# Performance work log

Measured on AMD Instinct MI355X. Metric: run time of the kernel, lower is better.

## Reference

```python
import jax, jax.numpy as jnp
import numpy as np

DIM = 768
HEADS = 12
EXPERTS = 8
HID = 3072  # dim * moe_mlp_ratio(=4)
TOP_K = 2
LN_EPS = 1e-5


def _layer_norm(x, g, b):
    mu = x.mean(-1, keepdims=True)
    var = ((x - mu) ** 2).mean(-1, keepdims=True)
    return (x - mu) * jax.lax.rsqrt(var + LN_EPS) * g + b


def setup_inputs() -> dict:
    key = jax.random.key(0)
    ks = jax.random.split(key, 16)
    s = 0.02
    return {
        "x": jax.random.normal(ks[0], (8, 196, DIM), jnp.float32),
        "ln1_g": jnp.ones((DIM,), jnp.float32),
        "ln1_b": jnp.zeros((DIM,), jnp.float32),
        "qkv_w": jax.random.normal(ks[1], (DIM, 3 * DIM), jnp.float32) * s,
        "qkv_b": jnp.zeros((3 * DIM,), jnp.float32),
        "proj_w": jax.random.normal(ks[2], (DIM, DIM), jnp.float32) * s,
        "proj_b": jnp.zeros((DIM,), jnp.float32),
        "ln2_g": jnp.ones((DIM,), jnp.float32),
        "ln2_b": jnp.zeros((DIM,), jnp.float32),
        "gate_w": jax.random.normal(ks[3], (DIM, EXPERTS), jnp.float32) * s,
        "w1": jax.random.normal(ks[4], (EXPERTS, DIM, HID), jnp.float32) * s,
        "b1": jnp.zeros((EXPERTS, HID), jnp.float32),
        "w2": jax.random.normal(ks[5], (EXPERTS, HID, DIM), jnp.float32) * s,
        "b2": jnp.zeros((EXPERTS, DIM), jnp.float32),
    }


def _attention(x, qkv_w, qkv_b, proj_w, proj_b):
    B, N, C = x.shape
    hd = C // HEADS
    qkv = (x @ qkv_w + qkv_b).reshape(B, N, 3, HEADS, hd).transpose(2, 0, 3, 1, 4)
    q, k, v = qkv[0], qkv[1], qkv[2]  # [B,H,N,hd]
    attn = jax.nn.softmax(jnp.einsum("bhnd,bhmd->bhnm", q, k) * (hd ** -0.5), axis=-1)
    o = jnp.einsum("bhnm,bhmd->bhnd", attn, v).transpose(0, 2, 1, 3).reshape(B, N, C)
    return o @ proj_w + proj_b


def _moe_mlp(xn, gate_w, w1, b1, w2, b2):
    # xn: [T, D]; noisy top-k gate in eval mode (no noise)
    T = xn.shape[0]
    logits = xn @ gate_w                                   # [T, E]
    top_logits, top_idx = jax.lax.top_k(logits, TOP_K)     # [T, k]
    top_gates = jax.nn.softmax(top_logits, axis=-1)        # [T, k]
    gates = jnp.zeros((T, EXPERTS), xn.dtype).at[
        jnp.arange(T)[:, None], top_idx
    ].set(top_gates)                                       # [T, E] sparse combine weights
    # dense-masked expert compute (math identical to dispatch: gate=0 tokens contribute 0)
    h = jax.nn.gelu(jnp.einsum("td,edh->teh", xn, w1) + b1, approximate=False)
    y = jnp.einsum("teh,ehd->ted", h, w2) + b2             # [T, E, D]
    return jnp.einsum("ted,te->td", y, gates)


def reference(x, ln1_g, ln1_b, qkv_w, qkv_b, proj_w, proj_b,
              ln2_g, ln2_b, gate_w, w1, b1, w2, b2):
    B, N, C = x.shape
    x = x + _attention(_layer_norm(x, ln1_g, ln1_b), qkv_w, qkv_b, proj_w, proj_b)
    xn = _layer_norm(x, ln2_g, ln2_b).reshape(B * N, C)
    moe_out = _moe_mlp(xn, gate_w, w1, b1, w2, b2).reshape(B, N, C)
    return x + moe_out
```

## Files before the change

kernel.cpp:

```cpp
#include <hip/hip_runtime.h>
#include <hip/hip_bf16.h>
#include <math.h>

#define DIMC 768
#define HEADS 12
#define HD 64
#define EXPERTS 8
#define HID 3072
#define BB 8
#define NN 196
#define TT (BB*NN)
#define CAP_ROWS 4224
#define LN_EPS 1e-5f

typedef float f32x4_t __attribute__((ext_vector_type(4)));
typedef short bf16x8_t __attribute__((ext_vector_type(8)));
typedef unsigned short u16x8_t __attribute__((ext_vector_type(8)));

__device__ __forceinline__ unsigned short f2bf(float f) {
    unsigned int u = __float_as_uint(f);
    u += 0x7FFFu + ((u >> 16) & 1u);
    return (unsigned short)(u >> 16);
}
__device__ __forceinline__ float bf2f(unsigned short u) {
    return __uint_as_float(((unsigned int)u) << 16);
}

__device__ __forceinline__ void gl_lds16(const void* g, void* l) {
    __builtin_amdgcn_global_load_lds(
        (const __attribute__((address_space(1))) unsigned int*)g,
        (__attribute__((address_space(3))) unsigned int*)l, 16, 0, 0);
}

template<int GATE>
__global__ void ln_kernel_t(const float* __restrict__ x, const float* __restrict__ g,
                            const float* __restrict__ b,
                            unsigned short* __restrict__ out_hi,
                            unsigned short* __restrict__ out_lo,
                            const float* __restrict__ gw, int* __restrict__ tok_e,
                            float* __restrict__ tok_g, int* __restrict__ counts) {
    int t = blockIdx.x;
    const float* xr = x + (size_t)t * DIMC;
    int tid = threadIdx.x;
    float v0 = xr[tid], v1 = xr[tid + 256], v2 = xr[tid + 512];
    __shared__ float red[256];
    red[tid] = v0 + v1 + v2;
    __syncthreads();
    for (int off = 128; off > 0; off >>= 1) {
        if (tid < off) red[tid] += red[tid + off];
        __syncthreads();
    }
    float mu = red[0] * (1.0f / DIMC);
    __syncthreads();
    float d0 = v0 - mu, d1 = v1 - mu, d2 = v2 - mu;
    red[tid] = d0*d0 + d1*d1 + d2*d2;
    __syncthreads();
    for (int off = 128; off > 0; off >>= 1) {
        if (tid < off) red[tid] += red[tid + off];
        __syncthreads();
    }
    float rstd = rsqrtf(red[0] * (1.0f / DIMC) + LN_EPS);
    float o0 = d0 * rstd * g[tid]       + b[tid];
    float o1 = d1 * rstd * g[tid + 256] + b[tid + 256];
    float o2 = d2 * rstd * g[tid + 512] + b[tid + 512];
    {
        unsigned short* o = out_hi + (size_t)t * DIMC;
        unsigned short h0 = f2bf(o0), h1 = f2bf(o1), h2 = f2bf(o2);
        o[tid] = h0; o[tid + 256] = h1; o[tid + 512] = h2;
        if (out_lo) {
            unsigned short* ol = out_lo + (size_t)t * DIMC;
            ol[tid]       = f2bf(o0 - bf2f(h0));
            ol[tid + 256] = f2bf(o1 - bf2f(h1));
            ol[tid + 512] = f2bf(o2 - bf2f(h2));
        }
    }
    if (GATE) {
        float p[8];
        const float* g0r = gw + (size_t)tid * 8;
        const float* g1r = gw + ((size_t)tid + 256) * 8;
        const float* g2r = gw + ((size_t)tid + 512) * 8;
        #pragma unroll
        for (int e = 0; e < 8; ++e)
            p[e] = o0 * g0r[e] + o1 * g1r[e] + o2 * g2r[e];
        #pragma unroll
        for (int off = 32; off > 0; off >>= 1)
            #pragma unroll
            for (int e = 0; e < 8; ++e) p[e] += __shfl_xor(p[e], off, 64);
        __shared__ float redw[4][8];
        int lane = tid & 63, w = tid >> 6;
        if (lane == 0) {
            #pragma unroll
            for (int e = 0; e < 8; ++e) redw[w][e] = p[e];
        }
        __syncthreads();
        if (tid == 0) {
            float lg[8];
            #pragma unroll
            for (int e = 0; e < 8; ++e)
                lg[e] = redw[0][e] + redw[1][e] + redw[2][e] + redw[3][e];
            int e0 = 0; float l0 = lg[0];
            #pragma unroll
            for (int e = 1; e < 8; ++e) if (lg[e] > l0) { l0 = lg[e]; e0 = e; }
            int e1 = -1; float l1 = -3e38f;
            #pragma unroll
            for (int e = 0; e < 8; ++e) if (e != e0 && lg[e] > l1) { l1 = lg[e]; e1 = e; }
            float pp = expf(l1 - l0);
            float ga = 1.f / (1.f + pp);
            float gb = pp / (1.f + pp);
            tok_e[t*2] = e0; tok_e[t*2+1] = e1;
            tok_g[t*2] = ga; tok_g[t*2+1] = gb;
            atomicAdd(&counts[e0], 1);
            atomicAdd(&counts[e1], 1);
        }
    }
}

__global__ void attn_mfma_kernel(const float* __restrict__ qkv,
                                 unsigned short* __restrict__ ao_h,
                                 unsigned short* __restrict__ ao_l) {
    __shared__ char psb[64 * 896];
    __shared__ unsigned short QsH[64 * 64], QsL[64 * 64];
    __shared__ unsigned short KsH[64 * 64], KsL[64 * 64];

    int bh = blockIdx.x;
    int b = bh / HEADS, h = bh % HEADS;
    int q0 = blockIdx.y * 64;
    const float* base = qkv + (size_t)b * NN * 2304 + h * 64;

    int tid = threadIdx.x;
    int sr = tid >> 3, sq = tid & 7;
    int lane = tid & 63;
    int wid = tid >> 6;
    int wm = (wid >> 2) * 32;
    int wn = (wid & 3) * 16;
    int lrow = lane & 15;
    int lq = lane >> 4;
    int colb_base = lq * 16;

    {
        int r = sr;
        int n = q0 + r;
        float v[8] = {0.f,0.f,0.f,0.f,0.f,0.f,0.f,0.f};
        if (n < NN) {
            float4 a0 = *(const float4*)(base + (size_t)n * 2304 + sq * 8);
            float4 a1 = *(const float4*)(base + (size_t)n * 2304 + sq * 8 + 4);
            v[0]=a0.x; v[1]=a0.y; v[2]=a0.z; v[3]=a0.w;
            v[4]=a1.x; v[5]=a1.y; v[6]=a1.z; v[7]=a1.w;
        }
        u16x8_t hv, lv;
        #pragma unroll
        for (int t = 0; t < 8; ++t) {
            unsigned short hh = f2bf(v[t]);
            hv[t] = hh; lv[t] = f2bf(v[t] - bf2f(hh));
        }
        int off = r * 128 + ((sq * 16) ^ ((r & 7) << 4));
        *(u16x8_t*)((char*)QsH + off) = hv;
        *(u16x8_t*)((char*)QsL + off) = lv;
    }

    for (int kt = 0; kt < 4; ++kt) {
        int j0 = kt * 64;
        __syncthreads();
        {
            int r = sr;
            int n = j0 + r;
            float v[8] = {0.f,0.f,0.f,0.f,0.f,0.f,0.f,0.f};
            if (n < NN) {
                float4 a0 = *(const float4*)(base + (size_t)n * 2304 + 768 + sq * 8);
                float4 a1 = *(const float4*)(base + (size_t)n * 2304 + 768 + sq * 8 + 4);
                v[0]=a0.x; v[1]=a0.y; v[2]=a0.z; v[3]=a0.w;
                v[4]=a1.x; v[5]=a1.y; v[6]=a1.z; v[7]=a1.w;
            }
            u16x8_t hv, lv;
            #pragma unroll
            for (int t = 0; t < 8; ++t) {
                unsigned short hh = f2bf(v[t]);
                hv[t] = hh; lv[t] = f2bf(v[t] - bf2f(hh));
            }
            int off = r * 128 + ((sq * 16) ^ ((r & 7) << 4));
            *(u16x8_t*)((char*)KsH + off) = hv;
            *(u16x8_t*)((char*)KsL + off) = lv;
        }
        __syncthreads();

        f32x4_t acc[2] = {};
        #pragma unroll
        for (int kk = 0; kk < 2; ++kk) {
            int colb = kk * 64 + colb_base;
            bf16x8_t qh[2], ql[2], kh, kl;
            #pragma unroll
            for (int i = 0; i < 2; ++i) {
                int ra = wm + i * 16 + lrow;
                int oa = ra * 128 + (colb ^ ((ra & 7) << 4));
                qh[i] = *(const bf16x8_t*)((const char*)QsH + oa);
                ql[i] = *(const bf16x8_t*)((const char*)QsL + oa);
            }
            int rb = wn + lrow;
            int ob = rb * 128 + (colb ^ ((rb & 7) << 4));
            kh = *(const bf16x8_t*)((const char*)KsH + ob);
            kl = *(const bf16x8_t*)((const char*)KsL + ob);
            #pragma unroll
            for (int mi = 0; mi < 2; ++mi) {
                acc[mi] = __builtin_amdgcn_mfma_f32_16x16x32_bf16(qh[mi], kh, acc[mi], 0, 0, 0);
                acc[mi] = __builtin_amdgcn_mfma_f32_16x16x32_bf16(qh[mi], kl, acc[mi], 0, 0, 0);
                acc[mi] = __builtin_amdgcn_mfma_f32_16x16x32_bf16(ql[mi], kh, acc[mi], 0, 0, 0);
            }
        }
        int jc = j0 + wn + lrow;
        if (jc < 224) {
            #pragma unroll
            for (int mi = 0; mi < 2; ++mi) {
                #pragma unroll
                for (int j = 0; j < 4; ++j) {
                    int row = wm + mi * 16 + lq * 4 + j;
                    int s = (row & 7) ^ (row >> 3);
                    *(float*)(psb + row * 896 + ((jc * 4) ^ (s << 4))) = acc[mi][j] * 0.125f;
                }
            }
        }
    }
    __syncthreads();

    {
        int i = tid >> 3, l = tid & 7;
        int s = (i & 7) ^ (i >> 3);
        char* prow = psb + i * 896;
        float mx = -1e30f;
        for (int j = l; j < NN; j += 8) mx = fmaxf(mx, *(const float*)(prow + ((j * 4) ^ (s << 4))));
        mx = fmaxf(mx, __shfl_xor(mx, 1, 8));
        mx = fmaxf(mx, __shfl_xor(mx, 2, 8));
        mx = fmaxf(mx, __shfl_xor(mx, 4, 8));
        float sum = 0.f;
        for (int j = l; j < NN; j += 8) {
            float* pp = (float*)(prow + ((j * 4) ^ (s << 4)));
            float e = expf(*pp - mx); *pp = e; sum += e;
        }
        sum += __shfl_xor(sum, 1, 8);
        sum += __shfl_xor(sum, 2, 8);
        sum += __shfl_xor(sum, 4, 8);
        float inv = 1.f / sum;
        for (int j = l; j < NN; j += 8) {
            float* pp = (float*)(prow + ((j * 4) ^ (s << 4)));
            *pp *= inv;
        }
    }

    f32x4_t oacc[2] = {};
    for (int kt = 0; kt < 4; ++kt) {
        int j0 = kt * 64;
        __syncthreads();
        {
            int r = sr;
            int n = j0 + r;
            float v[8] = {0.f,0.f,0.f,0.f,0.f,0.f,0.f,0.f};
            if (n < NN) {
                float4 a0 = *(const float4*)(base + (size_t)n * 2304 + 1536 + sq * 8);
                float4 a1 = *(const float4*)(base + (size_t)n * 2304 + 1536 + sq * 8 + 4);
                v[0]=a0.x; v[1]=a0.y; v[2]=a0.z; v[3]=a0.w;
                v[4]=a1.x; v[5]=a1.y; v[6]=a1.z; v[7]=a1.w;
            }
            #pragma unroll
            for (int t = 0; t < 8; ++t) {
                int d = sq * 8 + t;
                int sw = ((d & 7) ^ (d >> 3)) << 4;
                unsigned short hh = f2bf(v[t]);
                int off = d * 128 + ((r * 2) ^ sw);
                *(unsigned short*)((char*)KsH + off) = hh;
                *(unsigned short*)((char*)KsL + off) = f2bf(v[t] - bf2f(hh));
            }
        }
        __syncthreads();

        int kkmax = (kt == 3) ? 1 : 2;
        for (int kk = 0; kk < kkmax; ++kk) {
            int colb = kk * 64 + colb_base;
            bf16x8_t pah[2], pal[2], vh, vl;
            #pragma unroll
            for (int i = 0; i < 2; ++i) {
                int ra = wm + i * 16 + lrow;
                int s = (ra & 7) ^ (ra >> 3);
                const char* prow = psb + ra * 896;
                int jb = (j0 + kk * 32 + lq * 8) * 4;
                float4 a0 = *(const float4*)(prow + (jb ^ (s << 4)));
                float4 a1 = *(const float4*)(prow + ((jb + 16) ^ (s << 4)));
                float vv[8] = {a0.x,a0.y,a0.z,a0.w,a1.x,a1.y,a1.z,a1.w};
                u16x8_t hv, lv;
                #pragma unroll
                for (int t = 0; t < 8; ++t) {
                    unsigned short hh = f2bf(vv[t]);
                    hv[t] = hh; lv[t] = f2bf(vv[t] - bf2f(hh));
                }
                pah[i] = *(bf16x8_t*)&hv;
                pal[i] = *(bf16x8_t*)&lv;
            }
            int rb = wn + lrow;
            int ob = rb * 128 + (colb ^ (((rb & 7) ^ (rb >> 3)) << 4));
            vh = *(const bf16x8_t*)((const char*)KsH + ob);
            vl = *(const bf16x8_t*)((const char*)KsL + ob);
            #pragma unroll
            for (int mi = 0; mi < 2; ++mi) {
                oacc[mi] = __builtin_amdgcn_mfma_f32_16x16x32_bf16(pah[mi], vh, oacc[mi], 0, 0, 0);
                oacc[mi] = __builtin_amdgcn_mfma_f32_16x16x32_bf16(pah[mi], vl, oacc[mi], 0, 0, 0);
                oacc[mi] = __builtin_amdgcn_mfma_f32_16x16x32_bf16(pal[mi], vh, oacc[mi], 0, 0, 0);
            }
        }
    }

    #pragma unroll
    for (int mi = 0; mi < 2; ++mi) {
        int col = h * 64 + wn + lrow;
        #pragma unroll
        for (int j = 0; j < 4; ++j) {
            int n = q0 + wm + mi * 16 + lq * 4 + j;
            if (n < NN) {
                float v = oacc[mi][j];
                unsigned short hh = f2bf(v);
                size_t o = (size_t)(b * NN + n) * DIMC + col;
                ao_h[o] = hh;
                ao_l[o] = f2bf(v - bf2f(hh));
            }
        }
    }
}

__global__ void init_kernel(int* __restrict__ counts, int* __restrict__ row2tok, int cap,
                            unsigned short* __restrict__ zrow) {
    int i = blockIdx.x * blockDim.x + threadIdx.x;
    if (i < 8) counts[i] = 0;
    if (i < 128) zrow[i] = 0;
    if (i < cap) row2tok[i] = -1;
}

__global__ void offsets_kernel(const int* __restrict__ counts, int* __restrict__ offsets,
                               int* __restrict__ cursor) {
    if (threadIdx.x == 0 && blockIdx.x == 0) {
        int off = 0;
        for (int e = 0; e < 8; ++e) {
            offsets[e] = off;
            cursor[e]  = off;
            off += ((counts[e] + 63) / 64) * 64;
        }
        offsets[8] = off;
    }
}

__global__ void fill_kernel(const int* __restrict__ tok_e, int* __restrict__ cursor,
                            int* __restrict__ row2tok, int* __restrict__ tok_row) {
    int t = blockIdx.x * blockDim.x + threadIdx.x;
    if (t >= TT) return;
    #pragma unroll
    for (int k = 0; k < 2; ++k) {
        int e = tok_e[t*2+k];
        int slot = atomicAdd(&cursor[e], 1);
        row2tok[slot] = t;
        tok_row[t*2+k] = slot;
    }
}

__global__ void transpose_bf16(const float* __restrict__ src, unsigned short* __restrict__ dst,
                               int R, int C) {
    __shared__ float tile[64][65];
    const float* s = src + (size_t)blockIdx.z * R * C;
    unsigned short* d = dst + (size_t)blockIdx.z * R * C;
    int c0 = blockIdx.x * 64, r0 = blockIdx.y * 64;
    int tid = threadIdx.x;
    int tr = tid >> 4;
    int tc = (tid & 15) * 4;
    #pragma unroll
    for (int p = 0; p < 4; ++p) {
        int r = tr + p * 16;
        const float4 v = *(const float4*)(s + (size_t)(r0 + r) * C + c0 + tc);
        tile[r][tc+0] = v.x; tile[r][tc+1] = v.y; tile[r][tc+2] = v.z; tile[r][tc+3] = v.w;
    }
    __syncthreads();
    #pragma unroll
    for (int p = 0; p < 4; ++p) {
        int c = tr + p * 16;
        ushort4 o;
        o.x = f2bf(tile[tc+0][c]);
        o.y = f2bf(tile[tc+1][c]);
        o.z = f2bf(tile[tc+2][c]);
        o.w = f2bf(tile[tc+3][c]);
        *(ushort4*)(d + (size_t)(c0 + c) * R + r0 + tc) = o;
    }
}

__global__ void transpose_split_bf16(const float* __restrict__ src,
                                     unsigned short* __restrict__ dh,
                                     unsigned short* __restrict__ dl, int R, int C) {
    __shared__ float tile[64][65];
    int c0 = blockIdx.x * 64, r0 = blockIdx.y * 64;
    int tid = threadIdx.x;
    int tr = tid >> 4;
    int tc = (tid & 15) * 4;
    #pragma unroll
    for (int p = 0; p < 4; ++p) {
        int r = tr + p * 16;
        const float4 v = *(const float4*)(src + (size_t)(r0 + r) * C + c0 + tc);
        tile[r][tc+0] = v.x; tile[r][tc+1] = v.y; tile[r][tc+2] = v.z; tile[r][tc+3] = v.w;
    }
    __syncthreads();
    #pragma unroll
    for (int p = 0; p < 4; ++p) {
        int c = tr + p * 16;
        ushort4 h, l;
        float v0 = tile[tc+0][c], v1 = tile[tc+1][c], v2 = tile[tc+2][c], v3 = tile[tc+3][c];
        h.x = f2bf(v0); l.x = f2bf(v0 - bf2f(h.x));
        h.y = f2bf(v1); l.y = f2bf(v1 - bf2f(h.y));
        h.z = f2bf(v2); l.z = f2bf(v2 - bf2f(h.z));
        h.w = f2bf(v3); l.w = f2bf(v3 - bf2f(h.w));
        size_t off = (size_t)(c0 + c) * R + r0 + tc;
        *(ushort4*)(dh + off) = h;
        *(ushort4*)(dl + off) = l;
    }
}

template<int RES>
__global__ void mfma_gemm_split(const unsigned short* __restrict__ Ah,
                                const unsigned short* __restrict__ Al,
                                const unsigned short* __restrict__ Bth,
                                const unsigned short* __restrict__ Btl,
                                const float* __restrict__ bias,
                                const float* __restrict__ res,
                                float* __restrict__ C,
                                const unsigned short* __restrict__ zrow,
                                int M, int N, int K) {
    __shared__ unsigned short AsH[64 * 64];
    __shared__ unsigned short AsL[64 * 64];
    __shared__ unsigned short BsH[64 * 64];
    __shared__ unsigned short BsL[64 * 64];

    int m0 = blockIdx.x * 64;
    int n0 = blockIdx.y * 64;
    int tid = threadIdx.x;
    int lane = tid & 63;
    int wid = tid >> 6;
    int wm = (wid >> 1) * 32;
    int wn = (wid & 1) * 32;
    int colb_base = (lane >> 4) * 16;
    int lrow = lane & 15;

    f32x4_t acc[2][2] = {};

    for (int k0 = 0; k0 < K; k0 += 64) {
        #pragma unroll
        for (int p = 0; p < 2; ++p) {
            int s = tid + p * 256;
            int r = s >> 3, c = s & 7;
            int gc = c ^ (r & 7);
            bool inM = (m0 + r < M);
            size_t aoff = (size_t)(m0 + r) * K + k0 + gc * 8;
            gl_lds16(inM ? (const void*)(Ah + aoff) : (const void*)zrow, (char*)AsH + s * 16);
            gl_lds16(inM ? (const void*)(Al + aoff) : (const void*)zrow, (char*)AsL + s * 16);
            size_t boff = (size_t)(n0 + r) * K + k0 + gc * 8;
            gl_lds16((const void*)(Bth + boff), (char*)BsH + s * 16);
            gl_lds16((const void*)(Btl + boff), (char*)BsL + s * 16);
        }
        __syncthreads();
        #pragma unroll
        for (int kk = 0; kk < 2; ++kk) {
            int colb = kk * 64 + colb_base;
            bf16x8_t ah[2], al[2], bh[2], bl[2];
            #pragma unroll
            for (int i = 0; i < 2; ++i) {
                int ra = wm + i * 16 + lrow;
                int oa = ra * 128 + (colb ^ ((ra & 7) << 4));
                ah[i] = *(const bf16x8_t*)((const char*)AsH + oa);
                al[i] = *(const bf16x8_t*)((const char*)AsL + oa);
                int rb = wn + i * 16 + lrow;
                int ob = rb * 128 + (colb ^ ((rb & 7) << 4));
                bh[i] = *(const bf16x8_t*)((const char*)BsH + ob);
                bl[i] = *(const bf16x8_t*)((const char*)BsL + ob);
            }
            #pragma unroll
            for (int mi = 0; mi < 2; ++mi)
                #pragma unroll
                for (int ni = 0; ni < 2; ++ni) {
                    acc[mi][ni] = __builtin_amdgcn_mfma_f32_16x16x32_bf16(
                        ah[mi], bh[ni], acc[mi][ni], 0, 0, 0);
                    acc[mi][ni] = __builtin_amdgcn_mfma_f32_16x16x32_bf16(
                        ah[mi], bl[ni], acc[mi][ni], 0, 0, 0);
                    acc[mi][ni] = __builtin_amdgcn_mfma_f32_16x16x32_bf16(
                        al[mi], bh[ni], acc[mi][ni], 0, 0, 0);
                }
        }
        __syncthreads();
    }

    #pragma unroll
    for (int mi = 0; mi < 2; ++mi) {
        #pragma unroll
        for (int ni = 0; ni < 2; ++ni) {
            int col = n0 + wn + ni * 16 + lrow;
            #pragma unroll
            for (int j = 0; j < 4; ++j) {
                int row = m0 + wm + mi * 16 + (lane >> 4) * 4 + j;
                if (row < M) {
                    float v = acc[mi][ni][j] + bias[col];
                    if (RES) v += res[(size_t)row * N + col];
                    C[(size_t)row * N + col] = v;
                }
            }
        }
    }
}

template<int GATHER, int GELU, int OUT_BF16>
__global__ void mfma_gemm_grouped(const unsigned short* __restrict__ A,
                                  const unsigned short* __restrict__ Bt,
                                  const float* __restrict__ bias,
                                  const int* __restrict__ offsets,
                                  const int* __restrict__ row2tok,
                                  void* __restrict__ Cout,
                                  const unsigned short* __restrict__ zrow,
                                  int N, int K, int nxb) {
    __shared__ unsigned short As[64 * 64];
    __shared__ unsigned short Bs[128 * 64];
    __shared__ int toks[64];

    int nwg = gridDim.x;
    int pbid = blockIdx.x;
    int q = nwg >> 3, r8 = nwg & 7;
    int xcd = pbid & 7, slot = pbid >> 3;
    int L = (xcd < r8) ? xcd * (q + 1) + slot
                       : r8 * (q + 1) + (xcd - r8) * q + slot;
    int xb = L % nxb;
    int n0 = (L / nxb) * 128;
    int r0 = xb * 64;
    if (r0 >= offsets[8]) return;
    int e = 0;
    while (r0 >= offsets[e + 1]) ++e;

    int tid = threadIdx.x;
    if (GATHER && tid < 64) toks[tid] = row2tok[r0 + tid];
    __syncthreads();

    const unsigned short* Be = Bt + (size_t)e * N * K;

    int lane = tid & 63;
    int wid = tid >> 6;
    int wm = (wid >> 1) * 32;
    int wn = (wid & 1) * 64;
    int colb_base = (lane >> 4) * 16;
    int lrow = lane & 15;

    f32x4_t acc[2][4] = {};

    for (int k0 = 0; k0 < K; k0 += 64) {
        #pragma unroll
        for (int p = 0; p < 2; ++p) {
            int s = tid + p * 256;
            int r = s >> 3, c = s & 7;
            int gc = c ^ (r & 7);
            const void* asrc;
            if (GATHER) {
                int tok = toks[r];
                asrc = (tok >= 0) ? (const void*)(A + (size_t)tok * K + k0 + gc * 8)
                                  : (const void*)zrow;
            } else {
                asrc = (const void*)(A + (size_t)(r0 + r) * K + k0 + gc * 8);
            }
            gl_lds16(asrc, (char*)As + s * 16);
        }
        #pragma unroll
        for (int p = 0; p < 4; ++p) {
            int s = tid + p * 256;
            int r = s >> 3, c = s & 7;
            int gc = c ^ (r & 7);
            gl_lds16((const void*)(Be + (size_t)(n0 + r) * K + k0 + gc * 8),
                     (char*)Bs + s * 16);
        }
        __syncthreads();
        #pragma unroll
        for (int kk = 0; kk < 2; ++kk) {
            int colb = kk * 64 + colb_base;
            bf16x8_t a[2], b[4];
            #pragma unroll
            for (int i = 0; i < 2; ++i) {
                int ra = wm + i * 16 + lrow;
                a[i] = *(const bf16x8_t*)((const char*)As + ra * 128 + (colb ^ ((ra & 7) << 4)));
            }
            #pragma unroll
            for (int i = 0; i < 4; ++i) {
                int rb = wn + i * 16 + lrow;
                b[i] = *(const bf16x8_t*)((const char*)Bs + rb * 128 + (colb ^ ((rb & 7) << 4)));
            }
            #pragma unroll
            for (int mi = 0; mi < 2; ++mi)
                #pragma unroll
                for (int ni = 0; ni < 4; ++ni)
                    acc[mi][ni] = __builtin_amdgcn_mfma_f32_16x16x32_bf16(
                        a[mi], b[ni], acc[mi][ni], 0, 0, 0);
        }
        __syncthreads();
    }

    #pragma unroll
    for (int mi = 0; mi < 2; ++mi) {
        #pragma unroll
        for (int ni = 0; ni < 4; ++ni) {
            int col = n0 + wn + ni * 16 + lrow;
            float bv = GELU ? bias[(size_t)e * N + col] : 0.f;
            #pragma unroll
            for (int j = 0; j < 4; ++j) {
                int row = r0 + wm + mi * 16 + (lane >> 4) * 4 + j;
                float v = acc[mi][ni][j] + bv;
                if (GELU) v = 0.5f * v * (1.f + erff(v * 0.70710678f));
                if (OUT_BF16)
                    ((unsigned short*)Cout)[(size_t)row * N + col] = f2bf(v);
                else
                    ((float*)Cout)[(size_t)row * N + col] = v;
            }
        }
    }
}

__global__ void combine_kernel(const float* __restrict__ x_res, const float* __restrict__ y,
                               const float* __restrict__ b2, const int* __restrict__ tok_e,
                               const float* __restrict__ tok_g, const int* __restrict__ tok_row,
                               float* __restrict__ out) {
    int t = blockIdx.x;
    int c = blockIdx.y * 256 + threadIdx.x;
    int e0 = tok_e[t*2], e1 = tok_e[t*2+1];
    float g0 = tok_g[t*2], g1 = tok_g[t*2+1];
    int r0 = tok_row[t*2], r1 = tok_row[t*2+1];
    float v = x_res[(size_t)t * DIMC + c]
            + g0 * (y[(size_t)r0 * DIMC + c] + b2[(size_t)e0 * DIMC + c])
            + g1 * (y[(size_t)r1 * DIMC + c] + b2[(size_t)e1 * DIMC + c]);
    out[(size_t)t * DIMC + c] = v;
}

extern "C" void kernel_launch(void* const* d_in, const int* in_sizes, int n_in,
                              void* d_out, int out_size, void* d_ws, size_t ws_size,
                              hipStream_t stream) {
    const float* x      = (const float*)d_in[0];
    const float* ln1_g  = (const float*)d_in[1];
    const float* ln1_b  = (const float*)d_in[2];
    const float* qkv_w  = (const float*)d_in[3];
    const float* qkv_b  = (const float*)d_in[4];
    const float* proj_w = (const float*)d_in[5];
    const float* proj_b = (const float*)d_in[6];
    const float* ln2_g  = (const float*)d_in[7];
    const float* ln2_b  = (const float*)d_in[8];
    const float* gate_w = (const float*)d_in[9];
    const float* w1     = (const float*)d_in[10];
    const float* b1     = (const float*)d_in[11];
    const float* w2     = (const float*)d_in[12];
    const float* b2     = (const float*)d_in[13];
    float* out = (float*)d_out;

    char* p = (char*)d_ws;
    auto alloc = [&](size_t nbytes) {
        void* r = (void*)p;
        p += (nbytes + 255) & ~(size_t)255;
        return r;
    };
    unsigned short* xn1_h   = (unsigned short*)alloc((size_t)TT * DIMC * 2);
    unsigned short* xn1_l   = (unsigned short*)alloc((size_t)TT * DIMC * 2);
    float*          qkv     = (float*)alloc((size_t)TT * 2304 * 4);
    unsigned short* ao_h    = (unsigned short*)alloc((size_t)TT * DIMC * 2);
    unsigned short* ao_l    = (unsigned short*)alloc((size_t)TT * DIMC * 2);
    float*          x_res   = (float*)alloc((size_t)TT * DIMC * 4);
    unsigned short* xn2_bf  = (unsigned short*)alloc((size_t)TT * DIMC * 2);
    unsigned short* h       = (unsigned short*)alloc((size_t)CAP_ROWS * HID * 2);
    float*          y       = (float*)alloc((size_t)CAP_ROWS * DIMC * 4);
    unsigned short* w1t     = (unsigned short*)alloc((size_t)EXPERTS * DIMC * HID * 2);
    unsigned short* w2t     = (unsigned short*)alloc((size_t)EXPERTS * DIMC * HID * 2);
    unsigned short* qwt_h   = (unsigned short*)alloc((size_t)DIMC * 2304 * 2);
    unsigned short* qwt_l   = (unsigned short*)alloc((size_t)DIMC * 2304 * 2);
    unsigned short* pwt_h   = (unsigned short*)alloc((size_t)DIMC * DIMC * 2);
    unsigned short* pwt_l   = (unsigned short*)alloc((size_t)DIMC * DIMC * 2);
    float*          tok_g   = (float*)alloc((size_t)2 * TT * 4);
    int*            tok_e   = (int*)alloc((size_t)2 * TT * 4);
    int*            tok_row = (int*)alloc((size_t)2 * TT * 4);
    int*            row2tok = (int*)alloc((size_t)CAP_ROWS * 4);
    unsigned short* zrow    = (unsigned short*)alloc(256);
    int*            counts  = (int*)alloc(32 * 4);
    int*            offsets = (int*)alloc(32 * 4);
    int*            cursor  = (int*)alloc(32 * 4);

    init_kernel<<<(CAP_ROWS + 255) / 256, 256, 0, stream>>>(counts, row2tok, CAP_ROWS, zrow);

    transpose_bf16<<<dim3(HID / 64, DIMC / 64, EXPERTS), 256, 0, stream>>>(w1, w1t, DIMC, HID);
    transpose_bf16<<<dim3(DIMC / 64, HID / 64, EXPERTS), 256, 0, stream>>>(w2, w2t, HID, DIMC);
    transpose_split_bf16<<<dim3(2304 / 64, DIMC / 64), 256, 0, stream>>>(qkv_w, qwt_h, qwt_l,
                                                                         DIMC, 2304);
    transpose_split_bf16<<<dim3(DIMC / 64, DIMC / 64), 256, 0, stream>>>(proj_w, pwt_h, pwt_l,
                                                                         DIMC, DIMC);

    ln_kernel_t<0><<<TT, 256, 0, stream>>>(x, ln1_g, ln1_b, xn1_h, xn1_l,
                                           nullptr, nullptr, nullptr, nullptr);

    mfma_gemm_split<0><<<dim3((TT + 63) / 64, 2304 / 64), 256, 0, stream>>>(
        xn1_h, xn1_l, qwt_h, qwt_l, qkv_b, nullptr, qkv, zrow, TT, 2304, DIMC);

    attn_mfma_kernel<<<dim3(BB * HEADS, 4), 512, 0, stream>>>(qkv, ao_h, ao_l);

    mfma_gemm_split<1><<<dim3((TT + 63) / 64, DIMC / 64), 256, 0, stream>>>(
        ao_h, ao_l, pwt_h, pwt_l, proj_b, x, x_res, zrow, TT, DIMC, DIMC);

    ln_kernel_t<1><<<TT, 256, 0, stream>>>(x_res, ln2_g, ln2_b, xn2_bf, nullptr,
                                           gate_w, tok_e, tok_g, counts);

    offsets_kernel<<<1, 64, 0, stream>>>(counts, offsets, cursor);

    fill_kernel<<<(TT + 255) / 256, 256, 0, stream>>>(tok_e, cursor, row2tok, tok_row);

    {
        int nxb = CAP_ROWS / 64;
        int nwg1 = (HID / 128) * nxb;
        mfma_gemm_grouped<1, 1, 1><<<nwg1, 256, 0, stream>>>(
            xn2_bf, w1t, b1, offsets, row2tok, h, zrow, HID, DIMC, nxb);

        int nwg2 = (DIMC / 128) * nxb;
        mfma_gemm_grouped<0, 0, 0><<<nwg2, 256, 0, stream>>>(
            h, w2t, nullptr, offsets, row2tok, y, zrow, DIMC, HID, nxb);
    }

    combine_kernel<<<dim3(TT, 3), 256, 0, stream>>>(x_res, y, b2, tok_e, tok_g, tok_row, out);
}
```

Measured before the change: 272.7 us.

## Fuse expert weight transpose/bf16 conversion into grouped GEMM loads; XCD-remap split GEMMs

Removes the two separate transpose_bf16 passes over the expert weights (8x768x3072 fp32 each) and the bf16 transposed copies. The grouped MoE GEMMs now read the fp32 weights directly, convert them to bf16 and write them into the swizzled LDS tile in registers. The split-precision dense GEMMs also switch to a 1D grid with XCD-aware block remapping. The trade-off is that the expert GEMMs now load twice the bytes per B tile, and each active expert tile is reconverted by every row block instead of once.

```diff
diff --git a/kernel.cpp b/kernel.cpp
--- a/kernel.cpp
+++ b/kernel.cpp
@@ -30,6 +30,13 @@
     __builtin_amdgcn_global_load_lds(
         (const __attribute__((address_space(1))) unsigned int*)g,
         (__attribute__((address_space(3))) unsigned int*)l, 16, 0, 0);
+}
+
+__device__ __forceinline__ int xcd_remap(int pbid, int nwg) {
+    int q = nwg >> 3, r8 = nwg & 7;
+    int xcd = pbid & 7, slot = pbid >> 3;
+    return (xcd < r8) ? xcd * (q + 1) + slot
+                      : r8 * (q + 1) + (xcd - r8) * q + slot;
 }
 
 template<int GATE>
@@ -357,34 +364,6 @@
     }
 }
 
-__global__ void transpose_bf16(const float* __restrict__ src, unsigned short* __restrict__ dst,
-                               int R, int C) {
-    __shared__ float tile[64][65];
-    const float* s = src + (size_t)blockIdx.z * R * C;
-    unsigned short* d = dst + (size_t)blockIdx.z * R * C;
-    int c0 = blockIdx.x * 64, r0 = blockIdx.y * 64;
-    int tid = threadIdx.x;
-    int tr = tid >> 4;
-    int tc = (tid & 15) * 4;
-    #pragma unroll
-    for (int p = 0; p < 4; ++p) {
-        int r = tr + p * 16;
-        const float4 v = *(const float4*)(s + (size_t)(r0 + r) * C + c0 + tc);
-        tile[r][tc+0] = v.x; tile[r][tc+1] = v.y; tile[r][tc+2] = v.z; tile[r][tc+3] = v.w;
-    }
-    __syncthreads();
-    #pragma unroll
-    for (int p = 0; p < 4; ++p) {
-        int c = tr + p * 16;
-        ushort4 o;
-        o.x = f2bf(tile[tc+0][c]);
-        o.y = f2bf(tile[tc+1][c]);
-        o.z = f2bf(tile[tc+2][c]);
-        o.w = f2bf(tile[tc+3][c]);
-        *(ushort4*)(d + (size_t)(c0 + c) * R + r0 + tc) = o;
-    }
-}
-
 __global__ void transpose_split_bf16(const float* __restrict__ src,
                                      unsigned short* __restrict__ dh,
                                      unsigned short* __restrict__ dl, int R, int C) {
@@ -424,14 +403,15 @@
                                 const float* __restrict__ res,
                                 float* __restrict__ C,
                                 const unsigned short* __restrict__ zrow,
-                                int M, int N, int K) {
+                                int M, int N, int K, int nmb) {
     __shared__ unsigned short AsH[64 * 64];
     __shared__ unsigned short AsL[64 * 64];
     __shared__ unsigned short BsH[64 * 64];
     __shared__ unsigned short BsL[64 * 64];
 
-    int m0 = blockIdx.x * 64;
-    int n0 = blockIdx.y * 64;
+    int L = xcd_remap(blockIdx.x, gridDim.x);
+    int m0 = (L % nmb) * 64;
+    int n0 = (L / nmb) * 64;
     int tid = threadIdx.x;
     int lane = tid & 63;
     int wid = tid >> 6;
@@ -507,7 +487,7 @@
 
 template<int GATHER, int GELU, int OUT_BF16>
 __global__ void mfma_gemm_grouped(const unsigned short* __restrict__ A,
-                                  const unsigned short* __restrict__ Bt,
+                                  const float* __restrict__ W,
                                   const float* __restrict__ bias,
                                   const int* __restrict__ offsets,
                                   const int* __restrict__ row2tok,
@@ -518,12 +498,7 @@
     __shared__ unsigned short Bs[128 * 64];
     __shared__ int toks[64];
 
-    int nwg = gridDim.x;
-    int pbid = blockIdx.x;
-    int q = nwg >> 3, r8 = nwg & 7;
-    int xcd = pbid & 7, slot = pbid >> 3;
-    int L = (xcd < r8) ? xcd * (q + 1) + slot
-                       : r8 * (q + 1) + (xcd - r8) * q + slot;
+    int L = xcd_remap(blockIdx.x, gridDim.x);
     int xb = L % nxb;
     int n0 = (L / nxb) * 128;
     int r0 = xb * 64;
@@ -535,7 +510,7 @@
     if (GATHER && tid < 64) toks[tid] = row2tok[r0 + tid];
     __syncthreads();
 
-    const unsigned short* Be = Bt + (size_t)e * N * K;
+    const float* We = W + (size_t)e * K * N;
 
     int lane = tid & 63;
     int wid = tid >> 6;
@@ -563,12 +538,24 @@
             gl_lds16(asrc, (char*)As + s * 16);
         }
         #pragma unroll
-        for (int p = 0; p < 4; ++p) {
-            int s = tid + p * 256;
-            int r = s >> 3, c = s & 7;
-            int gc = c ^ (r & 7);
-            gl_lds16((const void*)(Be + (size_t)(n0 + r) * K + k0 + gc * 8),
-                     (char*)Bs + s * 16);
+        for (int p = 0; p < 2; ++p) {
+            int idx = tid + p * 256;
+            int k2 = idx & 31;
+            int nc = idx >> 5;
+            const float* w0 = We + (size_t)(k0 + 2 * k2) * N + n0 + nc * 8;
+            float4 a0 = *(const float4*)(w0);
+            float4 a1 = *(const float4*)(w0 + 4);
+            float4 b0 = *(const float4*)(w0 + N);
+            float4 b1 = *(const float4*)(w0 + N + 4);
+            float ka[8] = {a0.x,a0.y,a0.z,a0.w,a1.x,a1.y,a1.z,a1.w};
+            float kb[8] = {b0.x,b0.y,b0.z,b0.w,b1.x,b1.y,b1.z,b1.w};
+            #pragma unroll
+            for (int i = 0; i < 8; ++i) {
+                int n = nc * 8 + i;
+                unsigned int pk = (unsigned int)f2bf(ka[i]) |
+                                  ((unsigned int)f2bf(kb[i]) << 16);
+                *(unsigned int*)((char*)Bs + n * 128 + ((k2 * 4) ^ ((n & 7) << 4))) = pk;
+            }
         }
         __syncthreads();
         #pragma unroll
@@ -664,8 +651,6 @@
     unsigned short* xn2_bf  = (unsigned short*)alloc((size_t)TT * DIMC * 2);
     unsigned short* h       = (unsigned short*)alloc((size_t)CAP_ROWS * HID * 2);
     float*          y       = (float*)alloc((size_t)CAP_ROWS * DIMC * 4);
-    unsigned short* w1t     = (unsigned short*)alloc((size_t)EXPERTS * DIMC * HID * 2);
-    unsigned short* w2t     = (unsigned short*)alloc((size_t)EXPERTS * DIMC * HID * 2);
     unsigned short* qwt_h   = (unsigned short*)alloc((size_t)DIMC * 2304 * 2);
     unsigned short* qwt_l   = (unsigned short*)alloc((size_t)DIMC * 2304 * 2);
     unsigned short* pwt_h   = (unsigned short*)alloc((size_t)DIMC * DIMC * 2);
@@ -681,8 +666,6 @@
 
     init_kernel<<<(CAP_ROWS + 255) / 256, 256, 0, stream>>>(counts, row2tok, CAP_ROWS, zrow);
 
-    transpose_bf16<<<dim3(HID / 64, DIMC / 64, EXPERTS), 256, 0, stream>>>(w1, w1t, DIMC, HID);
-    transpose_bf16<<<dim3(DIMC / 64, HID / 64, EXPERTS), 256, 0, stream>>>(w2, w2t, HID, DIMC);
     transpose_split_bf16<<<dim3(2304 / 64, DIMC / 64), 256, 0, stream>>>(qkv_w, qwt_h, qwt_l,
                                                                          DIMC, 2304);
     transpose_split_bf16<<<dim3(DIMC / 64, DIMC / 64), 256, 0, stream>>>(proj_w, pwt_h, pwt_l,
@@ -691,13 +674,21 @@
     ln_kernel_t<0><<<TT, 256, 0, stream>>>(x, ln1_g, ln1_b, xn1_h, xn1_l,
                                            nullptr, nullptr, nullptr, nullptr);
 
-    mfma_gemm_split<0><<<dim3((TT + 63) / 64, 2304 / 64), 256, 0, stream>>>(
-        xn1_h, xn1_l, qwt_h, qwt_l, qkv_b, nullptr, qkv, zrow, TT, 2304, DIMC);
+    {
+        int nmb = (TT + 63) / 64;
+        int nwg = nmb * (2304 / 64);
+        mfma_gemm_split<0><<<nwg, 256, 0, stream>>>(
+            xn1_h, xn1_l, qwt_h, qwt_l, qkv_b, nullptr, qkv, zrow, TT, 2304, DIMC, nmb);
+    }
 
     attn_mfma_kernel<<<dim3(BB * HEADS, 4), 512, 0, stream>>>(qkv, ao_h, ao_l);
 
-    mfma_gemm_split<1><<<dim3((TT + 63) / 64, DIMC / 64), 256, 0, stream>>>(
-        ao_h, ao_l, pwt_h, pwt_l, proj_b, x, x_res, zrow, TT, DIMC, DIMC);
+    {
+        int nmb = (TT + 63) / 64;
+        int nwg = nmb * (DIMC / 64);
+        mfma_gemm_split<1><<<nwg, 256, 0, stream>>>(
+            ao_h, ao_l, pwt_h, pwt_l, proj_b, x, x_res, zrow, TT, DIMC, DIMC, nmb);
+    }
 
     ln_kernel_t<1><<<TT, 256, 0, stream>>>(x_res, ln2_g, ln2_b, xn2_bf, nullptr,
                                            gate_w, tok_e, tok_g, counts);
@@ -710,11 +701,11 @@
         int nxb = CAP_ROWS / 64;
         int nwg1 = (HID / 128) * nxb;
         mfma_gemm_grouped<1, 1, 1><<<nwg1, 256, 0, stream>>>(
-            xn2_bf, w1t, b1, offsets, row2tok, h, zrow, HID, DIMC, nxb);
+            xn2_bf, w1, b1, offsets, row2tok, h, zrow, HID, DIMC, nxb);
 
         int nwg2 = (DIMC / 128) * nxb;
         mfma_gemm_grouped<0, 0, 0><<<nwg2, 256, 0, stream>>>(
-            h, w2t, nullptr, offsets, row2tok, y, zrow, DIMC, HID, nxb);
+            h, w2, nullptr, offsets, row2tok, y, zrow, DIMC, HID, nxb);
     }
 
     combine_kernel<<<dim3(TT, 3), 256, 0, stream>>>(x_res, y, b2, tok_e, tok_g, tok_row, out);
```

After: 377.5 us. 1.38x slower.

## Double-buffer LDS in grouped MoE GEMM and XCD-remap split GEMM grid

Applied to the files above, without the earlier changes.

The grouped expert GEMM now uses two LDS buffers and issues the async global-to-LDS loads for the next K tile before computing the current one, removing one barrier per iteration and overlapping loads with MFMA work. The split-precision QKV/proj GEMMs switch to a 1D grid with the same XCD-aware block remapping, so neighbouring tiles share an XCD's L2. This doubles LDS use in the grouped kernel (about 48KB), which may lower occupancy.

```diff
diff --git a/kernel.cpp b/kernel.cpp
--- a/kernel.cpp
+++ b/kernel.cpp
@@ -30,6 +30,13 @@
     __builtin_amdgcn_global_load_lds(
         (const __attribute__((address_space(1))) unsigned int*)g,
         (__attribute__((address_space(3))) unsigned int*)l, 16, 0, 0);
+}
+
+__device__ __forceinline__ int xcd_remap(int pbid, int nwg) {
+    int q = nwg >> 3, r8 = nwg & 7;
+    int xcd = pbid & 7, slot = pbid >> 3;
+    return (xcd < r8) ? xcd * (q + 1) + slot
+                      : r8 * (q + 1) + (xcd - r8) * q + slot;
 }
 
 template<int GATE>
@@ -424,14 +431,15 @@
                                 const float* __restrict__ res,
                                 float* __restrict__ C,
                                 const unsigned short* __restrict__ zrow,
-                                int M, int N, int K) {
+                                int M, int N, int K, int nmb) {
     __shared__ unsigned short AsH[64 * 64];
     __shared__ unsigned short AsL[64 * 64];
     __shared__ unsigned short BsH[64 * 64];
     __shared__ unsigned short BsL[64 * 64];
 
-    int m0 = blockIdx.x * 64;
-    int n0 = blockIdx.y * 64;
+    int L = xcd_remap(blockIdx.x, gridDim.x);
+    int m0 = (L % nmb) * 64;
+    int n0 = (L / nmb) * 64;
     int tid = threadIdx.x;
     int lane = tid & 63;
     int wid = tid >> 6;
@@ -514,16 +522,11 @@
                                   void* __restrict__ Cout,
                                   const unsigned short* __restrict__ zrow,
                                   int N, int K, int nxb) {
-    __shared__ unsigned short As[64 * 64];
-    __shared__ unsigned short Bs[128 * 64];
+    __shared__ unsigned short As[2][64 * 64];
+    __shared__ unsigned short Bs[2][128 * 64];
     __shared__ int toks[64];
 
-    int nwg = gridDim.x;
-    int pbid = blockIdx.x;
-    int q = nwg >> 3, r8 = nwg & 7;
-    int xcd = pbid & 7, slot = pbid >> 3;
-    int L = (xcd < r8) ? xcd * (q + 1) + slot
-                       : r8 * (q + 1) + (xcd - r8) * q + slot;
+    int L = xcd_remap(blockIdx.x, gridDim.x);
     int xb = L % nxb;
     int n0 = (L / nxb) * 128;
     int r0 = xb * 64;
@@ -546,7 +549,7 @@
 
     f32x4_t acc[2][4] = {};
 
-    for (int k0 = 0; k0 < K; k0 += 64) {
+    auto stage = [&](int buf, int k0) {
         #pragma unroll
         for (int p = 0; p < 2; ++p) {
             int s = tid + p * 256;
@@ -560,7 +563,7 @@
             } else {
                 asrc = (const void*)(A + (size_t)(r0 + r) * K + k0 + gc * 8);
             }
-            gl_lds16(asrc, (char*)As + s * 16);
+            gl_lds16(asrc, (char*)As[buf] + s * 16);
         }
         #pragma unroll
         for (int p = 0; p < 4; ++p) {
@@ -568,9 +571,16 @@
             int r = s >> 3, c = s & 7;
             int gc = c ^ (r & 7);
             gl_lds16((const void*)(Be + (size_t)(n0 + r) * K + k0 + gc * 8),
-                     (char*)Bs + s * 16);
-        }
-        __syncthreads();
+                     (char*)Bs[buf] + s * 16);
+        }
+    };
+
+    stage(0, 0);
+    __syncthreads();
+
+    int cur = 0;
+    for (int k0 = 0; k0 < K; k0 += 64) {
+        if (k0 + 64 < K) stage(cur ^ 1, k0 + 64);
         #pragma unroll
         for (int kk = 0; kk < 2; ++kk) {
             int colb = kk * 64 + colb_base;
@@ -578,12 +588,12 @@
             #pragma unroll
             for (int i = 0; i < 2; ++i) {
                 int ra = wm + i * 16 + lrow;
-                a[i] = *(const bf16x8_t*)((const char*)As + ra * 128 + (colb ^ ((ra & 7) << 4)));
+                a[i] = *(const bf16x8_t*)((const char*)As[cur] + ra * 128 + (colb ^ ((ra & 7) << 4)));
             }
             #pragma unroll
             for (int i = 0; i < 4; ++i) {
                 int rb = wn + i * 16 + lrow;
-                b[i] = *(const bf16x8_t*)((const char*)Bs + rb * 128 + (colb ^ ((rb & 7) << 4)));
+                b[i] = *(const bf16x8_t*)((const char*)Bs[cur] + rb * 128 + (colb ^ ((rb & 7) << 4)));
             }
             #pragma unroll
             for (int mi = 0; mi < 2; ++mi)
@@ -593,6 +603,7 @@
                         a[mi], b[ni], acc[mi][ni], 0, 0, 0);
         }
         __syncthreads();
+        cur ^= 1;
     }
 
     #pragma unroll
@@ -691,13 +702,21 @@
     ln_kernel_t<0><<<TT, 256, 0, stream>>>(x, ln1_g, ln1_b, xn1_h, xn1_l,
                                            nullptr, nullptr, nullptr, nullptr);
 
-    mfma_gemm_split<0><<<dim3((TT + 63) / 64, 2304 / 64), 256, 0, stream>>>(
-        xn1_h, xn1_l, qwt_h, qwt_l, qkv_b, nullptr, qkv, zrow, TT, 2304, DIMC);
+    {
+        int nmb = (TT + 63) / 64;
+        int nwg = nmb * (2304 / 64);
+        mfma_gemm_split<0><<<nwg, 256, 0, stream>>>(
+            xn1_h, xn1_l, qwt_h, qwt_l, qkv_b, nullptr, qkv, zrow, TT, 2304, DIMC, nmb);
+    }
 
     attn_mfma_kernel<<<dim3(BB * HEADS, 4), 512, 0, stream>>>(qkv, ao_h, ao_l);
 
-    mfma_gemm_split<1><<<dim3((TT + 63) / 64, DIMC / 64), 256, 0, stream>>>(
-        ao_h, ao_l, pwt_h, pwt_l, proj_b, x, x_res, zrow, TT, DIMC, DIMC);
+    {
+        int nmb = (TT + 63) / 64;
+        int nwg = nmb * (DIMC / 64);
+        mfma_gemm_split<1><<<nwg, 256, 0, stream>>>(
+            ao_h, ao_l, pwt_h, pwt_l, proj_b, x, x_res, zrow, TT, DIMC, DIMC, nmb);
+    }
 
     ln_kernel_t<1><<<TT, 256, 0, stream>>>(x_res, ln2_g, ln2_b, xn2_bf, nullptr,
                                            gate_w, tok_e, tok_g, counts);
```

Measured after the change: 277.1 us. No clear change (+1.6%).
